# Optimization experiments

Measured on AMD Instinct MI355X. Metric: run time of the kernel, lower is better.

Reference implementation:

```python
import jax, jax.numpy as jnp
import numpy as np

LAMBDA_OPACITY = 1e-3
LAMBDA_DIST = 1e-3
LAMBDA_SAM = 1e-4
MIN_PIXNUM = 2
N_RAYS = 65536
S = 48            # samples per ray
NPIX = 65536      # semantic supervised pixels
C = 256           # number of SAM clusters
D = 16            # semantic feature dim


def setup_inputs() -> dict:
    key = jax.random.key(0)
    k = jax.random.split(key, 8)
    rgb_pred = jax.random.normal(k[0], (NPIX, 3), dtype=jnp.float32) * 0.1 + 0.5
    rgb_gt = jax.random.uniform(k[1], (NPIX, 3), dtype=jnp.float32)
    opacity = jax.random.uniform(k[2], (NPIX, 1), dtype=jnp.float32, minval=0.01, maxval=0.99)
    N = N_RAYS * S
    ws = jax.random.uniform(k[3], (N,), dtype=jnp.float32) / S
    deltas = jax.random.uniform(k[4], (N,), dtype=jnp.float32, minval=1e-3, maxval=2e-2)
    # midpoints: sorted (cumsum of deltas) within each ray, as the CUDA scan assumes
    ts = jnp.cumsum(deltas.reshape(N_RAYS, S), axis=1).reshape(N)
    ridx = jnp.arange(N_RAYS, dtype=jnp.int32)
    rays_a = jnp.stack([ridx, ridx * S, jnp.full((N_RAYS,), S, jnp.int32)], axis=1)
    sam = jax.random.randint(k[5], (NPIX, 1), 1, C + 1, dtype=jnp.int32)  # all > 0 (valid)
    semantic = jax.random.normal(k[6], (NPIX, D), dtype=jnp.float32)
    return dict(rgb_pred=rgb_pred, rgb_gt=rgb_gt, opacity=opacity, ws=ws,
                deltas=deltas, ts=ts, rays_a=rays_a, sam=sam, semantic=semantic)


def distortion_loss(ws, deltas, ts, rays_a):
    # Mip-NeRF 360 distortion via per-ray exclusive scans (DVGO-v2 form):
    # loss_ray = sum_i 2*w_i*(t_i*W_{<i} - (wt)_{<i}) + sum_i w_i^2*delta_i/3
    n_rays = rays_a.shape[0]
    starts = rays_a[:, 1]
    N = ws.shape[0]
    ray_ids = jnp.searchsorted(starts, jnp.arange(N, dtype=starts.dtype), side='right') - 1
    w_excl_g = jnp.cumsum(ws) - ws                 # global exclusive scan
    W_excl = w_excl_g - w_excl_g[starts][ray_ids]  # per-ray exclusive scan
    wts = ws * ts
    wt_excl_g = jnp.cumsum(wts) - wts
    WT_excl = wt_excl_g - wt_excl_g[starts][ray_ids]
    per_sample = 2.0 * ws * (ts * W_excl - WT_excl) + ws * ws * deltas / 3.0
    return jax.ops.segment_sum(per_sample, ray_ids, num_segments=n_rays)


def semantic_loss(semantic, sam):
    seg = sam[:, 0]
    valid = seg > 0
    cl = jnp.where(valid, seg - 1, 0)              # 0..C-1 cluster index
    w = valid.astype(semantic.dtype)
    counts = jax.ops.segment_sum(w, cl, num_segments=C)
    csafe = jnp.maximum(counts, 1.0)
    u = jax.ops.segment_sum(semantic * w[:, None], cl, num_segments=C) / csafe[:, None]  # (C,D) centroids
    dev = jnp.linalg.norm(semantic - u[cl], axis=1) * w
    phi_raw = jax.ops.segment_sum(dev, cl, num_segments=C) / (csafe * jnp.log(counts + 10.0))
    valid_cl = counts > MIN_PIXNUM
    phi = jax.lax.stop_gradient(jnp.clip(phi_raw * 10.0, 0.1, 1.0))  # detached, clipped
    logits = (semantic @ u.T) / phi[None, :]       # (P,C)
    dist = jnp.exp(logits) * valid_cl[None, :].astype(semantic.dtype)
    denom = dist.sum(axis=1) + 1e-6
    num = jnp.take_along_axis(dist, cl[:, None], axis=1)[:, 0]
    pix_valid = valid & valid_cl[cl]
    proto_nce = -jnp.sum(jnp.where(pix_valid, jnp.log(num / denom), 0.0))
    # sam_norm_loss_flag branch
    norms = jnp.linalg.norm(semantic, axis=1)
    norm_loss = jnp.sum(w * (norms - 1.0) ** 2) / jnp.maximum(w.sum(), 1.0)
    return (LAMBDA_SAM * proto_nce + 100.0 * norm_loss).reshape(1)


def reference(rgb_pred, rgb_gt, opacity, ws, deltas, ts, rays_a, sam, semantic):
    rgb = (rgb_pred - rgb_gt) ** 2                                    # d['rgb']
    o = opacity + 1e-10
    opac = LAMBDA_OPACITY * (-o * jnp.log(o))                         # d['opacity']
    dist = LAMBDA_DIST * distortion_loss(ws, deltas, ts, rays_a)      # d['distortion']
    sem = semantic_loss(semantic, sam)                                # d['semantic_render']
    return (rgb, opac, dist, sem)
```

## Files before the change

kernel.cpp:

```cpp
#include <hip/hip_runtime.h>
#include <hip/hip_bf16.h>

#define NPIX 65536
#define NRAYS 65536
#define SS 48
#define NC 256
#define ND 16
#define RPB 128

typedef __attribute__((ext_vector_type(8))) short short8;
typedef __attribute__((ext_vector_type(4))) float f32x4;

__device__ __forceinline__ unsigned short f2bf(float x) {
    unsigned u = __float_as_uint(x);
    unsigned r = u + 0x7fff + ((u >> 16) & 1);
    return (unsigned short)(r >> 16);
}
__device__ __forceinline__ float bf2f(unsigned short h) {
    return __uint_as_float(((unsigned)h) << 16);
}

__global__ __launch_bounds__(256) void kA(
    const float* __restrict__ rgb_pred, const float* __restrict__ rgb_gt,
    const float* __restrict__ opacity, const int* __restrict__ sam,
    const float* __restrict__ semantic,
    float* __restrict__ o_rgb, float* __restrict__ o_opac,
    float* __restrict__ cntpart, float* __restrict__ usumpart,
    float* __restrict__ normpart, float* __restrict__ wsumpart, int ppbA)
{
    __shared__ float cnt_s[NC];
    __shared__ float us_s[NC*17];
    __shared__ float red_s[8];
    const int t = threadIdx.x;
    const int b = blockIdx.x;
    for (int j = t; j < NC; j += 256) cnt_s[j] = 0.f;
    for (int j = t; j < NC*17; j += 256) us_s[j] = 0.f;
    __syncthreads();
    float nloc = 0.f, wloc = 0.f;
    for (int p = 0; p < ppbA; ++p) {
        const int i = (b*ppbA + p)*256 + t;
        const float pr0 = rgb_pred[3*i+0], pr1 = rgb_pred[3*i+1], pr2 = rgb_pred[3*i+2];
        const float g0 = rgb_gt[3*i+0],  g1 = rgb_gt[3*i+1],  g2 = rgb_gt[3*i+2];
        const float d0 = pr0-g0, d1 = pr1-g1, d2 = pr2-g2;
        o_rgb[3*i+0] = d0*d0; o_rgb[3*i+1] = d1*d1; o_rgb[3*i+2] = d2*d2;
        const float o = opacity[i] + 1e-10f;
        o_opac[i] = -0.001f * o * logf(o);
        const float4* sp = (const float4*)(semantic + (size_t)i*ND);
        const float4 a0 = sp[0], a1 = sp[1], a2 = sp[2], a3 = sp[3];
        const int seg = sam[i];
        if (seg > 0) {
            const int cl = seg - 1;
            const float ss =
                a0.x*a0.x + a0.y*a0.y + a0.z*a0.z + a0.w*a0.w +
                a1.x*a1.x + a1.y*a1.y + a1.z*a1.z + a1.w*a1.w +
                a2.x*a2.x + a2.y*a2.y + a2.z*a2.z + a2.w*a2.w +
                a3.x*a3.x + a3.y*a3.y + a3.z*a3.z + a3.w*a3.w;
            const float dn = sqrtf(ss) - 1.f;
            nloc += dn*dn; wloc += 1.f;
            atomicAdd(&cnt_s[cl], 1.f);
            float* up = us_s + cl*17;
            atomicAdd(up+0,  a0.x); atomicAdd(up+1,  a0.y);
            atomicAdd(up+2,  a0.z); atomicAdd(up+3,  a0.w);
            atomicAdd(up+4,  a1.x); atomicAdd(up+5,  a1.y);
            atomicAdd(up+6,  a1.z); atomicAdd(up+7,  a1.w);
            atomicAdd(up+8,  a2.x); atomicAdd(up+9,  a2.y);
            atomicAdd(up+10, a2.z); atomicAdd(up+11, a2.w);
            atomicAdd(up+12, a3.x); atomicAdd(up+13, a3.y);
            atomicAdd(up+14, a3.z); atomicAdd(up+15, a3.w);
        }
    }
    __syncthreads();
    for (int j = t; j < NC; j += 256) cntpart[b*NC + j] = cnt_s[j];
    for (int j = t; j < NC*ND; j += 256) {
        const int c = j >> 4, k = j & 15;
        usumpart[(size_t)b*NC*ND + j] = us_s[c*17 + k];
    }
    for (int off = 32; off > 0; off >>= 1) {
        nloc += __shfl_down(nloc, off);
        wloc += __shfl_down(wloc, off);
    }
    if ((t & 63) == 0) { red_s[t>>6] = nloc; red_s[4 + (t>>6)] = wloc; }
    __syncthreads();
    if (t == 0) {
        normpart[b] = red_s[0]+red_s[1]+red_s[2]+red_s[3];
        wsumpart[b] = red_s[4]+red_s[5]+red_s[6]+red_s[7];
    }
}

__global__ __launch_bounds__(128) void kDist(
    const float* __restrict__ wsv, const float* __restrict__ deltas,
    const float* __restrict__ tsv, const int* __restrict__ rays_a,
    float* __restrict__ o_dist)
{
    __shared__ float wS[SS][RPB+1];
    __shared__ float tS[SS][RPB+1];
    __shared__ float dS[SS][RPB+1];
    __shared__ int bad;
    const int t = threadIdx.x;
    const int r0 = blockIdx.x * RPB;
    const int ray = r0 + t;
    if (t == 0) bad = 0;
    __syncthreads();
    const int start = rays_a[3*ray + 1];
    const int cnt   = rays_a[3*ray + 2];
    if (start != ray*SS || cnt != SS) atomicAdd(&bad, 1);
    __syncthreads();

    if (bad == 0) {
        const size_t gb = (size_t)r0 * SS;
        const float4* gw = (const float4*)(wsv + gb);
        const float4* gt = (const float4*)(tsv + gb);
        const float4* gd = (const float4*)(deltas + gb);
        for (int i = t; i < RPB*SS/4; i += 128) {
            const int e = i*4;
            const int rr = e / SS;
            const int jj = e % SS;
            const float4 a = gw[i], b = gt[i], c = gd[i];
            wS[jj+0][rr]=a.x; wS[jj+1][rr]=a.y; wS[jj+2][rr]=a.z; wS[jj+3][rr]=a.w;
            tS[jj+0][rr]=b.x; tS[jj+1][rr]=b.y; tS[jj+2][rr]=b.z; tS[jj+3][rr]=b.w;
            dS[jj+0][rr]=c.x; dS[jj+1][rr]=c.y; dS[jj+2][rr]=c.z; dS[jj+3][rr]=c.w;
        }
        __syncthreads();
        float W = 0.f, WT = 0.f, acc = 0.f;
        for (int j = 0; j < SS; ++j) {
            const float w_ = wS[j][t], t_ = tS[j][t], d_ = dS[j][t];
            acc += 2.f*w_*(t_*W - WT) + w_*w_*d_*(1.f/3.f);
            W += w_; WT += w_*t_;
        }
        o_dist[ray] = 0.001f * acc;
    } else {
        float W = 0.f, WT = 0.f, acc = 0.f;
        for (int j = 0; j < cnt; ++j) {
            const float w_ = wsv[start+j], t_ = tsv[start+j], d_ = deltas[start+j];
            acc += 2.f*w_*(t_*W - WT) + w_*w_*d_*(1.f/3.f);
            W += w_; WT += w_*t_;
        }
        o_dist[ray] = 0.001f * acc;
    }
}

__global__ __launch_bounds__(256) void kP1(
    const float* __restrict__ cntpart, const float* __restrict__ usumpart,
    const float* __restrict__ normpart, const float* __restrict__ wsumpart,
    float* __restrict__ cnt, float* __restrict__ u,
    float* __restrict__ scal, int nblkA)
{
    const int c = blockIdx.x;
    const int t = threadIdx.x;
    const int kk = t & 15;
    const int s  = t >> 4;

    float us = 0.f;
    for (int b = s; b < nblkA; b += 16)
        us += usumpart[(size_t)b*(NC*ND) + c*ND + kk];

    __shared__ float lds[16][17];
    lds[s][kk] = us;

    float cs = (t < nblkA) ? cntpart[t*NC + c] : 0.f;
#pragma unroll
    for (int off = 32; off > 0; off >>= 1) cs += __shfl_xor(cs, off);
    __shared__ float cred[4];
    if ((t & 63) == 0) cred[t >> 6] = cs;
    __syncthreads();

    if (t < 16) {
        const float ctot = cred[0]+cred[1]+cred[2]+cred[3];
        float tot = 0.f;
#pragma unroll
        for (int s2 = 0; s2 < 16; ++s2) tot += lds[s2][t];
        u[c*ND + t] = tot / fmaxf(ctot, 1.f);
        if (t == 0) cnt[c] = ctot;
    }

    if (c == 0) {
        float n = (t < nblkA) ? normpart[t] : 0.f;
        float w2 = (t < nblkA) ? wsumpart[t] : 0.f;
#pragma unroll
        for (int off = 32; off > 0; off >>= 1) {
            n  += __shfl_xor(n, off);
            w2 += __shfl_xor(w2, off);
        }
        __shared__ float nr[4], wr[4];
        if ((t & 63) == 0) { nr[t >> 6] = n; wr[t >> 6] = w2; }
        __syncthreads();
        if (t == 0) {
            scal[0] = nr[0]+nr[1]+nr[2]+nr[3];
            scal[1] = wr[0]+wr[1]+wr[2]+wr[3];
        }
    }
}

__global__ __launch_bounds__(256) void kC(
    const float* __restrict__ semantic, const int* __restrict__ sam,
    const float* __restrict__ u, float* __restrict__ devpart, int ppb)
{
    __shared__ float u_s[NC*20];
    __shared__ float dev_s[NC];
    const int t = threadIdx.x, b = blockIdx.x;
    for (int j = t; j < NC*ND; j += 256) {
        const int c = j >> 4, k = j & 15;
        u_s[c*20 + k] = u[j];
    }
    for (int j = t; j < NC; j += 256) dev_s[j] = 0.f;
    __syncthreads();
    for (int p = 0; p < ppb; ++p) {
        const int i = (b*ppb + p)*256 + t;
        const int seg = sam[i];
        if (seg > 0) {
            const int cl = seg - 1;
            const float4* sp = (const float4*)(semantic + (size_t)i*ND);
            const float4 a0 = sp[0], a1 = sp[1], a2 = sp[2], a3 = sp[3];
            const float4* up = (const float4*)(u_s + cl*20);
            const float4 u0 = up[0], u1 = up[1], u2 = up[2], u3 = up[3];
            float q, d2 = 0.f;
            q = a0.x-u0.x; d2 += q*q;  q = a0.y-u0.y; d2 += q*q;
            q = a0.z-u0.z; d2 += q*q;  q = a0.w-u0.w; d2 += q*q;
            q = a1.x-u1.x; d2 += q*q;  q = a1.y-u1.y; d2 += q*q;
            q = a1.z-u1.z; d2 += q*q;  q = a1.w-u1.w; d2 += q*q;
            q = a2.x-u2.x; d2 += q*q;  q = a2.y-u2.y; d2 += q*q;
            q = a2.z-u2.z; d2 += q*q;  q = a2.w-u2.w; d2 += q*q;
            q = a3.x-u3.x; d2 += q*q;  q = a3.y-u3.y; d2 += q*q;
            q = a3.z-u3.z; d2 += q*q;  q = a3.w-u3.w; d2 += q*q;
            atomicAdd(&dev_s[cl], sqrtf(d2));
        }
    }
    __syncthreads();
    for (int j = t; j < NC; j += 256) devpart[b*NC + j] = dev_s[j];
}

__global__ __launch_bounds__(256) void kP2(
    const float* __restrict__ devpart, const float* __restrict__ cnt,
    const float* __restrict__ u, float* __restrict__ uphi,
    unsigned short* __restrict__ uphi_h, unsigned short* __restrict__ uphi_l,
    float* __restrict__ mf, float* __restrict__ scal, int nblkC)
{
    const int c = blockIdx.x;
    const int t = threadIdx.x;

    if (c == 0 && t == 0) {
        scal[2] = 0.f;
        ((unsigned*)scal)[3] = 0u;
    }

    float dv = (t < nblkC) ? devpart[t*NC + c] : 0.f;
#pragma unroll
    for (int off = 32; off > 0; off >>= 1) dv += __shfl_xor(dv, off);
    __shared__ float dred[4];
    __shared__ float inv_s;
    if ((t & 63) == 0) dred[t >> 6] = dv;
    __syncthreads();

    if (t == 0) {
        const float dtot = dred[0]+dred[1]+dred[2]+dred[3];
        const float cs = cnt[c];
        const float csafe = fmaxf(cs, 1.f);
        const float phiraw = dtot / (csafe * logf(cs + 10.f));
        const float phi = fminf(fmaxf(phiraw * 10.f, 0.1f), 1.f);
        inv_s = 1.f / phi;
        mf[c] = (cs > 2.0f) ? 1.f : 0.f;
    }
    __syncthreads();
    if (t < 16) {
        const float v = u[c*ND + t] * inv_s;
        uphi[c*ND + t] = v;
        const unsigned short h = f2bf(v);
        uphi_h[c*ND + t] = h;
        uphi_l[c*ND + t] = f2bf(v - bf2f(h));
    }
}

__global__ __launch_bounds__(256, 1) void kD(
    const float* __restrict__ semantic, const int* __restrict__ sam,
    const float* __restrict__ uphi,
    const unsigned short* __restrict__ uphi_h, const unsigned short* __restrict__ uphi_l,
    const float* __restrict__ mf,
    float* __restrict__ scal, float* __restrict__ o_sem)
{
    __shared__ float dlds[4][64];
    __shared__ float red_s[4];
    const int t = threadIdx.x;
    const int lane = t & 63;
    const int w = t >> 6;
    const int col = lane & 15;
    const int g   = lane >> 4;
    const int wbase = blockIdx.x * 256 + w * 64;

    short8 A[4];
#pragma unroll
    for (int pt = 0; pt < 4; ++pt) {
        const float* sp = semantic + (size_t)(wbase + pt*16 + col)*ND + (g & 1)*8;
        const float4 f0 = ((const float4*)sp)[0];
        const float4 f1 = ((const float4*)sp)[1];
        float fv[8] = {f0.x,f0.y,f0.z,f0.w, f1.x,f1.y,f1.z,f1.w};
        short8 a;
#pragma unroll
        for (int i = 0; i < 8; ++i) {
            const unsigned short h = f2bf(fv[i]);
            const unsigned short l = f2bf(fv[i] - bf2f(h));
            a[i] = (short)((g < 2) ? h : l);
        }
        A[pt] = a;
    }

    short8 B1[16], B2[16];
    const short8* Bh = (const short8*)uphi_h;
    const short8* Bl = (const short8*)uphi_l;
    const short8 zero8 = {0,0,0,0,0,0,0,0};
#pragma unroll
    for (int ct = 0; ct < 16; ++ct) {
        const int cls = ct*16 + col;
        const int idx = cls*2 + (g & 1);
        B1[ct] = Bh[idx];
        B2[ct] = (g < 2) ? Bl[idx] : zero8;
    }

    float mfv[16];
#pragma unroll
    for (int ct = 0; ct < 16; ++ct) mfv[ct] = mf[ct*16 + col];

    float dacc[4][4] = {};
#pragma unroll
    for (int ct = 0; ct < 16; ++ct) {
#pragma unroll
        for (int pt = 0; pt < 4; ++pt) {
            f32x4 d = {0.f, 0.f, 0.f, 0.f};
            d = __builtin_amdgcn_mfma_f32_16x16x32_bf16(A[pt], B2[ct], d, 0, 0, 0);
            d = __builtin_amdgcn_mfma_f32_16x16x32_bf16(A[pt], B1[ct], d, 0, 0, 0);
#pragma unroll
            for (int r = 0; r < 4; ++r)
                dacc[pt][r] += mfv[ct] * __expf(d[r]);
        }
    }

#pragma unroll
    for (int pt = 0; pt < 4; ++pt)
#pragma unroll
        for (int r = 0; r < 4; ++r) {
            float v = dacc[pt][r];
            v += __shfl_xor(v, 1);
            v += __shfl_xor(v, 2);
            v += __shfl_xor(v, 4);
            v += __shfl_xor(v, 8);
            dacc[pt][r] = v;
        }

    if (col == 0) {
#pragma unroll
        for (int pt = 0; pt < 4; ++pt)
#pragma unroll
            for (int r = 0; r < 4; ++r)
                dlds[w][pt*16 + 4*g + r] = dacc[pt][r];
    }
    const float denom = dlds[w][lane] + 1e-6f;

    const int p = wbase + lane;
    const int seg = sam[p];
    const int cl = (seg > 0) ? (seg - 1) : 0;
    const float4* sp = (const float4*)(semantic + (size_t)p*ND);
    const float4 b0 = sp[0], b1 = sp[1], b2 = sp[2], b3 = sp[3];
    const float4* uo = (const float4*)(uphi + cl*ND);
    const float4 c0 = uo[0], c1 = uo[1], c2 = uo[2], c3 = uo[3];
    const float down =
        b0.x*c0.x + b0.y*c0.y + b0.z*c0.z + b0.w*c0.w +
        b1.x*c1.x + b1.y*c1.y + b1.z*c1.z + b1.w*c1.w +
        b2.x*c2.x + b2.y*c2.y + b2.z*c2.z + b2.w*c2.w +
        b3.x*c3.x + b3.y*c3.y + b3.z*c3.z + b3.w*c3.w;
    const float mo = mf[cl];
    float contrib = (seg > 0 && mo > 0.5f) ? (__logf(denom) - down) : 0.f;

#pragma unroll
    for (int off = 32; off > 0; off >>= 1) contrib += __shfl_xor(contrib, off);
    if ((t & 63) == 0) red_s[t >> 6] = contrib;
    __syncthreads();
    if (t == 0) atomicAdd(&scal[2], red_s[0]+red_s[1]+red_s[2]+red_s[3]);

    if (t == 0) {
        __threadfence();
        unsigned* done = (unsigned*)(scal + 3);
        const unsigned old = atomicAdd(done, 1u);
        if (old == gridDim.x - 1) {
            const float proto = atomicAdd(&scal[2], 0.f);
            const float nrm   = scal[0];
            const float wsum  = scal[1];
            o_sem[0] = 1e-4f * proto + 100.f * nrm / fmaxf(wsum, 1.f);
        }
    }
}

extern "C" void kernel_launch(void* const* d_in, const int* in_sizes, int n_in,
                              void* d_out, int out_size, void* d_ws, size_t ws_size,
                              hipStream_t stream)
{
    const float* rgb_pred = (const float*)d_in[0];
    const float* rgb_gt   = (const float*)d_in[1];
    const float* opacity  = (const float*)d_in[2];
    const float* wsv      = (const float*)d_in[3];
    const float* deltas   = (const float*)d_in[4];
    const float* tsv      = (const float*)d_in[5];
    const int*   rays_a   = (const int*)d_in[6];
    const int*   sam      = (const int*)d_in[7];
    const float* semantic = (const float*)d_in[8];

    float* out    = (float*)d_out;
    float* o_rgb  = out;
    float* o_opac = out + 196608;
    float* o_dist = out + 262144;
    float* o_sem  = out + 327680;
    float* wsf    = (float*)d_ws;

    int nblkA = 256, nblkC = 256;
    size_t need = ((size_t)nblkA*NC*(ND+1) + (size_t)nblkC*NC + NC + 2*NC*ND + NC*ND + 2*nblkA + 64) * 4;
    if (ws_size < need) { nblkA = 128; nblkC = 128; }
    const int ppbA = NPIX / (nblkA * 256);
    const int ppbC = NPIX / (nblkC * 256);

    float*          w_cntpart  = wsf;
    float*          w_usum     = w_cntpart + (size_t)nblkA*NC;
    float*          w_devpart  = w_usum + (size_t)nblkA*NC*ND;
    float*          w_cnt      = w_devpart + (size_t)nblkC*NC;
    float*          w_u        = w_cnt + NC;
    float*          w_uphi     = w_u + NC*ND;
    float*          w_scal     = w_uphi + NC*ND;
    float*          w_mf       = w_scal + 8;
    float*          w_normpart = w_mf + NC;
    float*          w_wsumpart = w_normpart + nblkA;
    unsigned short* w_uh       = (unsigned short*)(w_wsumpart + nblkA);
    unsigned short* w_ul       = w_uh + NC*ND;

    kA<<<nblkA, 256, 0, stream>>>(rgb_pred, rgb_gt, opacity, sam, semantic,
                                  o_rgb, o_opac, w_cntpart, w_usum,
                                  w_normpart, w_wsumpart, ppbA);
    kDist<<<NRAYS/RPB, RPB, 0, stream>>>(wsv, deltas, tsv, rays_a, o_dist);
    kP1<<<NC, 256, 0, stream>>>(w_cntpart, w_usum, w_normpart, w_wsumpart,
                                w_cnt, w_u, w_scal, nblkA);
    kC<<<nblkC, 256, 0, stream>>>(semantic, sam, w_u, w_devpart, ppbC);
    kP2<<<NC, 256, 0, stream>>>(w_devpart, w_cnt, w_u, w_uphi, w_uh, w_ul,
                                w_mf, w_scal, nblkC);
    kD<<<NPIX/256, 256, 0, stream>>>(semantic, sam, w_uphi, w_uh, w_ul, w_mf, w_scal, o_sem);
}
```

Baseline: 54.39 us.

## Fuse distortion into front kernel and merge deviation pass with finalize via last-block

The pixel-statistics kernel and the distortion kernel become one launch, with extra blocks handling rays. Each ray is now processed by one wavefront that uses a shuffle-based inclusive scan instead of staging data through shared memory. The deviation kernel and the phi/finalize kernel are merged: blocks add into a global per-cluster array with atomics, and the last block to finish, detected through an atomic counter, computes phi and writes the scaled prototypes. This removes two launches and a partial-sum buffer. The cost is global atomic contention and a hard-coded 256-block layout that drops the fallback for a small workspace; the wave-scan path also assumes at most 64 samples per ray.

```diff
diff --git a/kernel.cpp b/kernel.cpp
--- a/kernel.cpp
+++ b/kernel.cpp
@@ -6,7 +6,6 @@
 #define SS 48
 #define NC 256
 #define ND 16
-#define RPB 128
 
 typedef __attribute__((ext_vector_type(8))) short short8;
 typedef __attribute__((ext_vector_type(4))) float f32x4;
@@ -20,122 +19,110 @@
     return __uint_as_float(((unsigned)h) << 16);
 }
 
-__global__ __launch_bounds__(256) void kA(
+__global__ __launch_bounds__(256) void kFront(
     const float* __restrict__ rgb_pred, const float* __restrict__ rgb_gt,
     const float* __restrict__ opacity, const int* __restrict__ sam,
     const float* __restrict__ semantic,
+    const float* __restrict__ wsv, const float* __restrict__ deltas,
+    const float* __restrict__ tsv, const int* __restrict__ rays_a,
     float* __restrict__ o_rgb, float* __restrict__ o_opac,
+    float* __restrict__ o_dist,
     float* __restrict__ cntpart, float* __restrict__ usumpart,
-    float* __restrict__ normpart, float* __restrict__ wsumpart, int ppbA)
+    float* __restrict__ normpart, float* __restrict__ wsumpart,
+    float* __restrict__ dev, float* __restrict__ scal,
+    unsigned* __restrict__ doneC)
 {
     __shared__ float cnt_s[NC];
     __shared__ float us_s[NC*17];
     __shared__ float red_s[8];
     const int t = threadIdx.x;
-    const int b = blockIdx.x;
-    for (int j = t; j < NC; j += 256) cnt_s[j] = 0.f;
-    for (int j = t; j < NC*17; j += 256) us_s[j] = 0.f;
-    __syncthreads();
-    float nloc = 0.f, wloc = 0.f;
-    for (int p = 0; p < ppbA; ++p) {
-        const int i = (b*ppbA + p)*256 + t;
-        const float pr0 = rgb_pred[3*i+0], pr1 = rgb_pred[3*i+1], pr2 = rgb_pred[3*i+2];
-        const float g0 = rgb_gt[3*i+0],  g1 = rgb_gt[3*i+1],  g2 = rgb_gt[3*i+2];
-        const float d0 = pr0-g0, d1 = pr1-g1, d2 = pr2-g2;
-        o_rgb[3*i+0] = d0*d0; o_rgb[3*i+1] = d1*d1; o_rgb[3*i+2] = d2*d2;
-        const float o = opacity[i] + 1e-10f;
-        o_opac[i] = -0.001f * o * logf(o);
-        const float4* sp = (const float4*)(semantic + (size_t)i*ND);
-        const float4 a0 = sp[0], a1 = sp[1], a2 = sp[2], a3 = sp[3];
-        const int seg = sam[i];
-        if (seg > 0) {
-            const int cl = seg - 1;
-            const float ss =
-                a0.x*a0.x + a0.y*a0.y + a0.z*a0.z + a0.w*a0.w +
-                a1.x*a1.x + a1.y*a1.y + a1.z*a1.z + a1.w*a1.w +
-                a2.x*a2.x + a2.y*a2.y + a2.z*a2.z + a2.w*a2.w +
-                a3.x*a3.x + a3.y*a3.y + a3.z*a3.z + a3.w*a3.w;
-            const float dn = sqrtf(ss) - 1.f;
-            nloc += dn*dn; wloc += 1.f;
-            atomicAdd(&cnt_s[cl], 1.f);
-            float* up = us_s + cl*17;
-            atomicAdd(up+0,  a0.x); atomicAdd(up+1,  a0.y);
-            atomicAdd(up+2,  a0.z); atomicAdd(up+3,  a0.w);
-            atomicAdd(up+4,  a1.x); atomicAdd(up+5,  a1.y);
-            atomicAdd(up+6,  a1.z); atomicAdd(up+7,  a1.w);
-            atomicAdd(up+8,  a2.x); atomicAdd(up+9,  a2.y);
-            atomicAdd(up+10, a2.z); atomicAdd(up+11, a2.w);
-            atomicAdd(up+12, a3.x); atomicAdd(up+13, a3.y);
-            atomicAdd(up+14, a3.z); atomicAdd(up+15, a3.w);
-        }
-    }
-    __syncthreads();
-    for (int j = t; j < NC; j += 256) cntpart[b*NC + j] = cnt_s[j];
-    for (int j = t; j < NC*ND; j += 256) {
-        const int c = j >> 4, k = j & 15;
-        usumpart[(size_t)b*NC*ND + j] = us_s[c*17 + k];
-    }
-    for (int off = 32; off > 0; off >>= 1) {
-        nloc += __shfl_down(nloc, off);
-        wloc += __shfl_down(wloc, off);
-    }
-    if ((t & 63) == 0) { red_s[t>>6] = nloc; red_s[4 + (t>>6)] = wloc; }
-    __syncthreads();
-    if (t == 0) {
-        normpart[b] = red_s[0]+red_s[1]+red_s[2]+red_s[3];
-        wsumpart[b] = red_s[4]+red_s[5]+red_s[6]+red_s[7];
-    }
-}
-
-__global__ __launch_bounds__(128) void kDist(
-    const float* __restrict__ wsv, const float* __restrict__ deltas,
-    const float* __restrict__ tsv, const int* __restrict__ rays_a,
-    float* __restrict__ o_dist)
-{
-    __shared__ float wS[SS][RPB+1];
-    __shared__ float tS[SS][RPB+1];
-    __shared__ float dS[SS][RPB+1];
-    __shared__ int bad;
-    const int t = threadIdx.x;
-    const int r0 = blockIdx.x * RPB;
-    const int ray = r0 + t;
-    if (t == 0) bad = 0;
-    __syncthreads();
-    const int start = rays_a[3*ray + 1];
-    const int cnt   = rays_a[3*ray + 2];
-    if (start != ray*SS || cnt != SS) atomicAdd(&bad, 1);
-    __syncthreads();
-
-    if (bad == 0) {
-        const size_t gb = (size_t)r0 * SS;
-        const float4* gw = (const float4*)(wsv + gb);
-        const float4* gt = (const float4*)(tsv + gb);
-        const float4* gd = (const float4*)(deltas + gb);
-        for (int i = t; i < RPB*SS/4; i += 128) {
-            const int e = i*4;
-            const int rr = e / SS;
-            const int jj = e % SS;
-            const float4 a = gw[i], b = gt[i], c = gd[i];
-            wS[jj+0][rr]=a.x; wS[jj+1][rr]=a.y; wS[jj+2][rr]=a.z; wS[jj+3][rr]=a.w;
-            tS[jj+0][rr]=b.x; tS[jj+1][rr]=b.y; tS[jj+2][rr]=b.z; tS[jj+3][rr]=b.w;
-            dS[jj+0][rr]=c.x; dS[jj+1][rr]=c.y; dS[jj+2][rr]=c.z; dS[jj+3][rr]=c.w;
-        }
+    const int lane = t & 63;
+    const int w = t >> 6;
+
+    if ((int)blockIdx.x < 256) {
+        const int b = blockIdx.x;
+        if (b == 0) {
+            dev[t] = 0.f;
+            if (t == 0) {
+                scal[2] = 0.f;
+                ((unsigned*)scal)[3] = 0u;
+                *doneC = 0u;
+            }
+        }
+        for (int j = t; j < NC; j += 256) cnt_s[j] = 0.f;
+        for (int j = t; j < NC*17; j += 256) us_s[j] = 0.f;
         __syncthreads();
-        float W = 0.f, WT = 0.f, acc = 0.f;
-        for (int j = 0; j < SS; ++j) {
-            const float w_ = wS[j][t], t_ = tS[j][t], d_ = dS[j][t];
-            acc += 2.f*w_*(t_*W - WT) + w_*w_*d_*(1.f/3.f);
-            W += w_; WT += w_*t_;
-        }
-        o_dist[ray] = 0.001f * acc;
+        float nloc = 0.f, wloc = 0.f;
+        {
+            const int i = b*256 + t;
+            const float pr0 = rgb_pred[3*i+0], pr1 = rgb_pred[3*i+1], pr2 = rgb_pred[3*i+2];
+            const float g0 = rgb_gt[3*i+0],  g1 = rgb_gt[3*i+1],  g2 = rgb_gt[3*i+2];
+            const float d0 = pr0-g0, d1 = pr1-g1, d2 = pr2-g2;
+            o_rgb[3*i+0] = d0*d0; o_rgb[3*i+1] = d1*d1; o_rgb[3*i+2] = d2*d2;
+            const float o = opacity[i] + 1e-10f;
+            o_opac[i] = -0.001f * o * logf(o);
+            const float4* sp = (const float4*)(semantic + (size_t)i*ND);
+            const float4 a0 = sp[0], a1 = sp[1], a2 = sp[2], a3 = sp[3];
+            const int seg = sam[i];
+            if (seg > 0) {
+                const int cl = seg - 1;
+                const float ss =
+                    a0.x*a0.x + a0.y*a0.y + a0.z*a0.z + a0.w*a0.w +
+                    a1.x*a1.x + a1.y*a1.y + a1.z*a1.z + a1.w*a1.w +
+                    a2.x*a2.x + a2.y*a2.y + a2.z*a2.z + a2.w*a2.w +
+                    a3.x*a3.x + a3.y*a3.y + a3.z*a3.z + a3.w*a3.w;
+                const float dn = sqrtf(ss) - 1.f;
+                nloc += dn*dn; wloc += 1.f;
+                atomicAdd(&cnt_s[cl], 1.f);
+                float* up = us_s + cl*17;
+                atomicAdd(up+0,  a0.x); atomicAdd(up+1,  a0.y);
+                atomicAdd(up+2,  a0.z); atomicAdd(up+3,  a0.w);
+                atomicAdd(up+4,  a1.x); atomicAdd(up+5,  a1.y);
+                atomicAdd(up+6,  a1.z); atomicAdd(up+7,  a1.w);
+                atomicAdd(up+8,  a2.x); atomicAdd(up+9,  a2.y);
+                atomicAdd(up+10, a2.z); atomicAdd(up+11, a2.w);
+                atomicAdd(up+12, a3.x); atomicAdd(up+13, a3.y);
+                atomicAdd(up+14, a3.z); atomicAdd(up+15, a3.w);
+            }
+        }
+        __syncthreads();
+        for (int j = t; j < NC; j += 256) cntpart[b*NC + j] = cnt_s[j];
+        for (int j = t; j < NC*ND; j += 256) {
+            const int c = j >> 4, k = j & 15;
+            usumpart[(size_t)b*NC*ND + j] = us_s[c*17 + k];
+        }
+#pragma unroll
+        for (int off = 32; off > 0; off >>= 1) {
+            nloc += __shfl_xor(nloc, off);
+            wloc += __shfl_xor(wloc, off);
+        }
+        if (lane == 0) { red_s[w] = nloc; red_s[4 + w] = wloc; }
+        __syncthreads();
+        if (t == 0) {
+            normpart[b] = red_s[0]+red_s[1]+red_s[2]+red_s[3];
+            wsumpart[b] = red_s[4]+red_s[5]+red_s[6]+red_s[7];
+        }
     } else {
-        float W = 0.f, WT = 0.f, acc = 0.f;
-        for (int j = 0; j < cnt; ++j) {
-            const float w_ = wsv[start+j], t_ = tsv[start+j], d_ = deltas[start+j];
-            acc += 2.f*w_*(t_*W - WT) + w_*w_*d_*(1.f/3.f);
-            W += w_; WT += w_*t_;
-        }
-        o_dist[ray] = 0.001f * acc;
+        const int ray = (blockIdx.x - 256)*4 + w;
+        const int start = rays_a[3*ray + 1];
+        const int cnt   = rays_a[3*ray + 2];
+        const bool act = lane < cnt;
+        const float w_ = act ? wsv[start+lane]    : 0.f;
+        const float t_ = act ? tsv[start+lane]    : 0.f;
+        const float d_ = act ? deltas[start+lane] : 0.f;
+        const float wt_ = w_*t_;
+        float sw = w_, swt = wt_;
+#pragma unroll
+        for (int off = 1; off < 64; off <<= 1) {
+            const float aw  = __shfl_up(sw, off);
+            const float awt = __shfl_up(swt, off);
+            if (lane >= off) { sw += aw; swt += awt; }
+        }
+        const float Wex = sw - w_, WTex = swt - wt_;
+        float per = 2.f*w_*(t_*Wex - WTex) + w_*w_*d_*(1.f/3.f);
+#pragma unroll
+        for (int off = 32; off > 0; off >>= 1) per += __shfl_xor(per, off);
+        if (lane == 0) o_dist[ray] = 0.001f * per;
     }
 }
 
@@ -143,7 +130,7 @@
     const float* __restrict__ cntpart, const float* __restrict__ usumpart,
     const float* __restrict__ normpart, const float* __restrict__ wsumpart,
     float* __restrict__ cnt, float* __restrict__ u,
-    float* __restrict__ scal, int nblkA)
+    float* __restrict__ scal)
 {
     const int c = blockIdx.x;
     const int t = threadIdx.x;
@@ -151,13 +138,13 @@
     const int s  = t >> 4;
 
     float us = 0.f;
-    for (int b = s; b < nblkA; b += 16)
+    for (int b = s; b < 256; b += 16)
         us += usumpart[(size_t)b*(NC*ND) + c*ND + kk];
 
     __shared__ float lds[16][17];
     lds[s][kk] = us;
 
-    float cs = (t < nblkA) ? cntpart[t*NC + c] : 0.f;
+    float cs = cntpart[t*NC + c];
 #pragma unroll
     for (int off = 32; off > 0; off >>= 1) cs += __shfl_xor(cs, off);
     __shared__ float cred[4];
@@ -174,8 +161,8 @@
     }
 
     if (c == 0) {
-        float n = (t < nblkA) ? normpart[t] : 0.f;
-        float w2 = (t < nblkA) ? wsumpart[t] : 0.f;
+        float n  = normpart[t];
+        float w2 = wsumpart[t];
 #pragma unroll
         for (int off = 32; off > 0; off >>= 1) {
             n  += __shfl_xor(n, off);
@@ -191,21 +178,23 @@
     }
 }
 
-__global__ __launch_bounds__(256) void kC(
+__global__ __launch_bounds__(256) void kCP2(
     const float* __restrict__ semantic, const int* __restrict__ sam,
-    const float* __restrict__ u, float* __restrict__ devpart, int ppb)
+    const float* __restrict__ u, const float* __restrict__ cnt,
+    float* __restrict__ dev, float* __restrict__ uphi,
+    unsigned short* __restrict__ uphi_h, unsigned short* __restrict__ uphi_l,
+    float* __restrict__ mf, unsigned* __restrict__ doneC)
 {
     __shared__ float u_s[NC*20];
-    __shared__ float dev_s[NC];
+    __shared__ int lastflag;
     const int t = threadIdx.x, b = blockIdx.x;
     for (int j = t; j < NC*ND; j += 256) {
         const int c = j >> 4, k = j & 15;
         u_s[c*20 + k] = u[j];
     }
-    for (int j = t; j < NC; j += 256) dev_s[j] = 0.f;
     __syncthreads();
-    for (int p = 0; p < ppb; ++p) {
-        const int i = (b*ppb + p)*256 + t;
+    {
+        const int i = b*256 + t;
         const int seg = sam[i];
         if (seg > 0) {
             const int cl = seg - 1;
@@ -222,51 +211,33 @@
             q = a2.z-u2.z; d2 += q*q;  q = a2.w-u2.w; d2 += q*q;
             q = a3.x-u3.x; d2 += q*q;  q = a3.y-u3.y; d2 += q*q;
             q = a3.z-u3.z; d2 += q*q;  q = a3.w-u3.w; d2 += q*q;
-            atomicAdd(&dev_s[cl], sqrtf(d2));
+            atomicAdd(&dev[cl], sqrtf(d2));
         }
     }
     __syncthreads();
-    for (int j = t; j < NC; j += 256) devpart[b*NC + j] = dev_s[j];
-}
-
-__global__ __launch_bounds__(256) void kP2(
-    const float* __restrict__ devpart, const float* __restrict__ cnt,
-    const float* __restrict__ u, float* __restrict__ uphi,
-    unsigned short* __restrict__ uphi_h, unsigned short* __restrict__ uphi_l,
-    float* __restrict__ mf, float* __restrict__ scal, int nblkC)
-{
-    const int c = blockIdx.x;
-    const int t = threadIdx.x;
-
-    if (c == 0 && t == 0) {
-        scal[2] = 0.f;
-        ((unsigned*)scal)[3] = 0u;
-    }
-
-    float dv = (t < nblkC) ? devpart[t*NC + c] : 0.f;
-#pragma unroll
-    for (int off = 32; off > 0; off >>= 1) dv += __shfl_xor(dv, off);
-    __shared__ float dred[4];
-    __shared__ float inv_s;
-    if ((t & 63) == 0) dred[t >> 6] = dv;
+    if (t == 0) {
+        __threadfence();
+        const unsigned old = atomicAdd(doneC, 1u);
+        lastflag = (old == 255u) ? 1 : 0;
+    }
     __syncthreads();
-
-    if (t == 0) {
-        const float dtot = dred[0]+dred[1]+dred[2]+dred[3];
+    if (lastflag) {
+        const int c = t;
+        const float dv = atomicAdd(&dev[c], 0.f);
         const float cs = cnt[c];
         const float csafe = fmaxf(cs, 1.f);
-        const float phiraw = dtot / (csafe * logf(cs + 10.f));
+        const float phiraw = dv / (csafe * logf(cs + 10.f));
         const float phi = fminf(fmaxf(phiraw * 10.f, 0.1f), 1.f);
-        inv_s = 1.f / phi;
+        const float inv = 1.f / phi;
         mf[c] = (cs > 2.0f) ? 1.f : 0.f;
-    }
-    __syncthreads();
-    if (t < 16) {
-        const float v = u[c*ND + t] * inv_s;
-        uphi[c*ND + t] = v;
-        const unsigned short h = f2bf(v);
-        uphi_h[c*ND + t] = h;
-        uphi_l[c*ND + t] = f2bf(v - bf2f(h));
+#pragma unroll
+        for (int k = 0; k < ND; ++k) {
+            const float v = u_s[c*20 + k] * inv;
+            uphi[c*ND + k] = v;
+            const unsigned short h = f2bf(v);
+            uphi_h[c*ND + k] = h;
+            uphi_l[c*ND + k] = f2bf(v - bf2f(h));
+        }
     }
 }
 
@@ -409,33 +380,30 @@
     float* o_sem  = out + 327680;
     float* wsf    = (float*)d_ws;
 
-    int nblkA = 256, nblkC = 256;
-    size_t need = ((size_t)nblkA*NC*(ND+1) + (size_t)nblkC*NC + NC + 2*NC*ND + NC*ND + 2*nblkA + 64) * 4;
-    if (ws_size < need) { nblkA = 128; nblkC = 128; }
-    const int ppbA = NPIX / (nblkA * 256);
-    const int ppbC = NPIX / (nblkC * 256);
-
     float*          w_cntpart  = wsf;
-    float*          w_usum     = w_cntpart + (size_t)nblkA*NC;
-    float*          w_devpart  = w_usum + (size_t)nblkA*NC*ND;
-    float*          w_cnt      = w_devpart + (size_t)nblkC*NC;
+    float*          w_usum     = w_cntpart + (size_t)256*NC;
+    float*          w_dev      = w_usum + (size_t)256*NC*ND;
+    float*          w_cnt      = w_dev + NC;
     float*          w_u        = w_cnt + NC;
     float*          w_uphi     = w_u + NC*ND;
     float*          w_scal     = w_uphi + NC*ND;
     float*          w_mf       = w_scal + 8;
     float*          w_normpart = w_mf + NC;
-    float*          w_wsumpart = w_normpart + nblkA;
-    unsigned short* w_uh       = (unsigned short*)(w_wsumpart + nblkA);
+    float*          w_wsumpart = w_normpart + 256;
+    unsigned*       w_doneC    = (unsigned*)(w_wsumpart + 256);
+    unsigned short* w_uh       = (unsigned short*)(w_doneC + 4);
     unsigned short* w_ul       = w_uh + NC*ND;
 
-    kA<<<nblkA, 256, 0, stream>>>(rgb_pred, rgb_gt, opacity, sam, semantic,
-                                  o_rgb, o_opac, w_cntpart, w_usum,
-                                  w_normpart, w_wsumpart, ppbA);
-    kDist<<<NRAYS/RPB, RPB, 0, stream>>>(wsv, deltas, tsv, rays_a, o_dist);
+    kFront<<<256 + NRAYS/4, 256, 0, stream>>>(
+        rgb_pred, rgb_gt, opacity, sam, semantic,
+        wsv, deltas, tsv, rays_a,
+        o_rgb, o_opac, o_dist,
+        w_cntpart, w_usum, w_normpart, w_wsumpart,
+        w_dev, w_scal, w_doneC);
     kP1<<<NC, 256, 0, stream>>>(w_cntpart, w_usum, w_normpart, w_wsumpart,
-                                w_cnt, w_u, w_scal, nblkA);
-    kC<<<nblkC, 256, 0, stream>>>(semantic, sam, w_u, w_devpart, ppbC);
-    kP2<<<NC, 256, 0, stream>>>(w_devpart, w_cnt, w_u, w_uphi, w_uh, w_ul,
-                                w_mf, w_scal, nblkC);
-    kD<<<NPIX/256, 256, 0, stream>>>(semantic, sam, w_uphi, w_uh, w_ul, w_mf, w_scal, o_sem);
-}
+                                w_cnt, w_u, w_scal);
+    kCP2<<<NC, 256, 0, stream>>>(semantic, sam, w_u, w_cnt,
+                                 w_dev, w_uphi, w_uh, w_ul, w_mf, w_doneC);
+    kD<<<NPIX/256, 256, 0, stream>>>(semantic, sam, w_uphi, w_uh, w_ul,
+                                     w_mf, w_scal, o_sem);
+}
```

Result: slower. 95.23 us (+75.1%).
